# Kernel tuning notes

Hardware: AMD Instinct MI355X
Metric: run time of the kernel (lower is better)

Reference implementation:

```python
import jax, jax.numpy as jnp
import numpy as np

POOL = 7          # cf.pool_size
SR = 2            # roi_align sampling_ratio
LEVELS = [0, 1, 2, 3]
C = 192           # cf.end_filts
HC = 2            # cf.head_classes
RF = 1
N_ROIS = 1000
B = 4


def roi_align_2d(fmap, boxes, batch_inds, pool_size=POOL, sr=SR):
    """Bilinear RoIAlign. fmap [B,C,H,W]; boxes [N,4] = (y1,x1,y2,x2) in fmap pixel coords."""
    _, _, H, W = fmap.shape
    y1, x1, y2, x2 = boxes[:, 0], boxes[:, 1], boxes[:, 2], boxes[:, 3]
    bin_h = jnp.maximum(y2 - y1, 1.0) / pool_size
    bin_w = jnp.maximum(x2 - x1, 1.0) / pool_size
    # sampling offsets within the roi, [pool*sr]
    grid = (jnp.arange(pool_size, dtype=jnp.float32)[:, None]
            + (jnp.arange(sr, dtype=jnp.float32)[None, :] + 0.5) / sr).reshape(-1)
    ys = y1[:, None] + grid[None, :] * bin_h[:, None]   # [N, P*S]
    xs = x1[:, None] + grid[None, :] * bin_w[:, None]   # [N, P*S]
    y = jnp.broadcast_to(ys[:, :, None], (ys.shape[0], ys.shape[1], xs.shape[1]))  # [N,PS,PS]
    x = jnp.broadcast_to(xs[:, None, :], y.shape)
    valid = (y >= -1.0) & (y <= H) & (x >= -1.0) & (x <= W)
    y = jnp.clip(y, 0.0, H - 1)
    x = jnp.clip(x, 0.0, W - 1)
    y0 = jnp.floor(y).astype(jnp.int32)
    x0 = jnp.floor(x).astype(jnp.int32)
    y1i = jnp.minimum(y0 + 1, H - 1)
    x1i = jnp.minimum(x0 + 1, W - 1)
    ly = y - y0
    lx = x - x0
    b = batch_inds[:, None, None]
    f00 = fmap[b, :, y0, x0]    # [N,PS,PS,C]
    f01 = fmap[b, :, y0, x1i]
    f10 = fmap[b, :, y1i, x0]
    f11 = fmap[b, :, y1i, x1i]
    w00 = ((1 - ly) * (1 - lx))[..., None]
    w01 = ((1 - ly) * lx)[..., None]
    w10 = (ly * (1 - lx))[..., None]
    w11 = (ly * lx)[..., None]
    val = (f00 * w00 + f01 * w01 + f10 * w10 + f11 * w11) * valid[..., None]
    n = val.shape[0]
    val = val.reshape(n, pool_size, sr, pool_size, sr, -1).mean(axis=(2, 4))  # [N,P,P,C]
    return jnp.transpose(val, (0, 3, 1, 2))  # [N,C,P,P]


def pyramid_roi_align(fmaps, rois, pool_size=POOL, levels=LEVELS):
    boxes = jax.lax.stop_gradient(rois[:, :4])  # level_boxes.detach() in original
    batch_ix = rois[:, 4].astype(jnp.int32)
    h = boxes[:, 2] - boxes[:, 0]
    w = boxes[:, 3] - boxes[:, 1]
    roi_level = jnp.clip(jnp.round(4.0 + jnp.log2(jnp.sqrt(h * w))),
                         levels[0], levels[-1]).astype(jnp.int32)
    pooled = jnp.zeros((boxes.shape[0], fmaps[0].shape[1], pool_size, pool_size), fmaps[0].dtype)
    for li, lvl in enumerate(levels):
        H, W = fmaps[li].shape[2], fmaps[li].shape[3]
        scale = jnp.asarray([H, W, H, W], jnp.float32)
        p = roi_align_2d(fmaps[li], boxes * scale, batch_ix, pool_size)
        pooled = jnp.where((roi_level == lvl)[:, None, None, None], p, pooled)
    return pooled


def setup_inputs() -> dict:
    key = jax.random.key(0)
    ks = jax.random.split(key, 20)
    fmap0 = jax.random.normal(ks[0], (B, C, 128, 128), jnp.float32)
    fmap1 = jax.random.normal(ks[1], (B, C, 64, 64), jnp.float32)
    fmap2 = jax.random.normal(ks[2], (B, C, 32, 32), jnp.float32)
    fmap3 = jax.random.normal(ks[3], (B, C, 16, 16), jnp.float32)
    # valid normalized rois: (y1,x1,y2,x2,batch_ix)
    cy = jax.random.uniform(ks[4], (N_ROIS,), minval=0.15, maxval=0.85)
    cx = jax.random.uniform(ks[5], (N_ROIS,), minval=0.15, maxval=0.85)
    hh = jax.random.uniform(ks[6], (N_ROIS,), minval=0.02, maxval=0.15)
    hw = jax.random.uniform(ks[7], (N_ROIS,), minval=0.02, maxval=0.15)
    bix = jax.random.randint(ks[8], (N_ROIS,), 0, B).astype(jnp.float32)
    rois = jnp.stack([jnp.clip(cy - hh, 0, 1), jnp.clip(cx - hw, 0, 1),
                      jnp.clip(cy + hh, 0, 1), jnp.clip(cx + hw, 0, 1), bix], axis=1)
    d = C * 4  # 768
    s1 = 1.0 / np.sqrt(C * POOL * POOL)
    s2 = 1.0 / np.sqrt(d)
    params = dict(
        w1=jax.random.normal(ks[9], (d, C, POOL, POOL), jnp.float32) * s1,
        b1=jnp.zeros((d,), jnp.float32),
        w2=jax.random.normal(ks[10], (d, d), jnp.float32) * s2,
        b2=jnp.zeros((d,), jnp.float32),
        w_bbox=jax.random.normal(ks[11], (HC * 4, d), jnp.float32) * s2,
        b_bbox=jnp.zeros((HC * 4,), jnp.float32),
        w_cls=jax.random.normal(ks[12], (HC, d), jnp.float32) * s2,
        b_cls=jnp.zeros((HC,), jnp.float32),
        w_reg=jax.random.normal(ks[13], (HC * RF, d), jnp.float32) * s2,
        b_reg=jnp.zeros((HC * RF,), jnp.float32),
        w_unc=jax.random.normal(ks[14], (HC, d), jnp.float32) * s2,
        b_unc=jnp.zeros((HC,), jnp.float32),
    )
    return dict(fmap0=fmap0, fmap1=fmap1, fmap2=fmap2, fmap3=fmap3, rois=rois, **params)


def reference(fmap0, fmap1, fmap2, fmap3, rois, w1, b1, w2, b2,
              w_bbox, b_bbox, w_cls, b_cls, w_reg, b_reg, w_unc, b_unc):
    x = pyramid_roi_align([fmap0, fmap1, fmap2, fmap3], rois)      # [N,C,7,7]
    x = jax.nn.relu(jnp.einsum('ncij,ocij->no', x, w1) + b1)       # conv1 ks=7 -> 1x1
    x = jax.nn.relu(x @ w2.T + b2)                                 # conv2 1x1
    n = x.shape[0]
    mrcnn_bbox = (x @ w_bbox.T + b_bbox).reshape(n, -1, 4)         # [N,HC,2*dim]
    mrcnn_class_logits = x @ w_cls.T + b_cls                       # [N,HC]
    reg = (x @ w_reg.T + b_reg).reshape(n, -1, RF)
    unc = x @ w_unc.T + b_unc
    mrcnn_regress = jnp.concatenate([reg, unc[..., None]], axis=2)  # [N,HC,RF+1]
    return mrcnn_bbox, mrcnn_class_logits, mrcnn_regress
```

## Files before the change

### kernel.cpp

```cpp
#include <hip/hip_runtime.h>
#include <hip/hip_bf16.h>
#include <cstddef>
#include <cstdint>

typedef __attribute__((ext_vector_type(8))) short short8;
typedef __attribute__((ext_vector_type(16))) float float16;

#define C_CH 192
#define PK   9408
#define D1   768

__device__ __forceinline__ ushort f2bf(float v) {
    return __builtin_bit_cast(unsigned short, __float2bfloat16(v));
}

__device__ __forceinline__ void gload16(const void* g, void* l) {
    __builtin_amdgcn_global_load_lds(
        (const __attribute__((address_space(1))) void*)g,
        (__attribute__((address_space(3))) void*)l, 16, 0, 0);
}

__global__ __launch_bounds__(256) void cvt_bf16_2(
    const float* __restrict__ in1, ushort* __restrict__ out1, int n4_1,
    const float* __restrict__ in2, ushort* __restrict__ out2, int n4_2)
{
    int i = blockIdx.x * 256 + threadIdx.x;
    const float* in; ushort* out;
    if (i < n4_1) { in = in1; out = out1; }
    else          { i -= n4_1; if (i >= n4_2) return; in = in2; out = out2; }
    float4 v = ((const float4*)in)[i];
    ushort4 o;
    o.x = f2bf(v.x); o.y = f2bf(v.y); o.z = f2bf(v.z); o.w = f2bf(v.w);
    ((ushort4*)out)[i] = o;
}

__global__ __launch_bounds__(256) void cvt_bf16(const float* __restrict__ in,
                                                ushort* __restrict__ out, int n4)
{
    int i = blockIdx.x * 256 + threadIdx.x;
    if (i >= n4) return;
    float4 v = ((const float4*)in)[i];
    ushort4 o;
    o.x = f2bf(v.x); o.y = f2bf(v.y); o.z = f2bf(v.z); o.w = f2bf(v.w);
    ((ushort4*)out)[i] = o;
}

__global__ __launch_bounds__(256) void fused_pre(
    const float* __restrict__ f0, const float* __restrict__ f1,
    const float* __restrict__ f2, const float* __restrict__ f3,
    ushort* __restrict__ o0, ushort* __restrict__ o1,
    ushort* __restrict__ o2, ushort* __restrict__ o3,
    const float* __restrict__ w1src, ushort* __restrict__ w1dst, int n41,
    const float* __restrict__ w2src, ushort* __restrict__ w2dst, int n42,
    int nTrans)
{
    __shared__ unsigned int sm[96][33];

    int bx = blockIdx.x;
    if (bx >= nTrans) {
        int i = (bx - nTrans) * 256 + threadIdx.x;
        const float* in; ushort* out;
        if (i < n41) { in = w1src; out = w1dst; }
        else         { i -= n41; if (i >= n42) return; in = w2src; out = w2dst; }
        float4 v = ((const float4*)in)[i];
        ushort4 o;
        o.x = f2bf(v.x); o.y = f2bf(v.y); o.z = f2bf(v.z); o.w = f2bf(v.w);
        ((ushort4*)out)[i] = o;
        return;
    }

    int b = bx / 680;
    int t = bx - b * 680;
    const float* in; ushort* out; int HW, hw0;
    if      (t < 512) { in = f0; out = o0; HW = 16384; hw0 = t * 32; }
    else if (t < 640) { in = f1; out = o1; HW = 4096;  hw0 = (t - 512) * 32; }
    else if (t < 672) { in = f2; out = o2; HW = 1024;  hw0 = (t - 640) * 32; }
    else              { in = f3; out = o3; HW = 256;   hw0 = (t - 672) * 32; }

    int tx = threadIdx.x & 31;
    int ty = threadIdx.x >> 5;

    const float* ip = in + (size_t)b * C_CH * HW + hw0;
    #pragma unroll
    for (int it = 0; it < 12; ++it) {
        int cp = it * 8 + ty;
        float v0 = ip[(size_t)(2 * cp)     * HW + tx];
        float v1 = ip[(size_t)(2 * cp + 1) * HW + tx];
        sm[cp][tx] = (unsigned int)f2bf(v0) | ((unsigned int)f2bf(v1) << 16);
    }
    __syncthreads();

    unsigned int* op = (unsigned int*)(out + ((size_t)b * HW + hw0) * C_CH);
    #pragma unroll
    for (int it = 0; it < 12; ++it) {
        int idx = it * 256 + (int)threadIdx.x;
        int r = idx / 96;
        int p = idx - r * 96;
        op[idx] = sm[p][r];
    }
}

__device__ __forceinline__ void issue8(
    const char* sbase, const int (*offB)[4], int s2, int c16, float4* u)
{
    #pragma unroll
    for (int k = 0; k < 8; ++k) {
        int s  = s2 + (k >> 2);
        int tp = k & 3;
        u[k] = *(const float4*)(sbase + (offB[s][tp] + c16));
    }
}

__device__ __forceinline__ void comp8(
    const float4* u, const float (*wt)[4], int s2, float* a)
{
    #pragma unroll
    for (int k = 0; k < 8; ++k) {
        float w = wt[s2 + (k >> 2)][k & 3];
        unsigned int u0 = __builtin_bit_cast(unsigned int, u[k].x);
        unsigned int u1 = __builtin_bit_cast(unsigned int, u[k].y);
        unsigned int u2 = __builtin_bit_cast(unsigned int, u[k].z);
        unsigned int u3 = __builtin_bit_cast(unsigned int, u[k].w);
        a[0] = fmaf(__builtin_bit_cast(float, u0 << 16),         w, a[0]);
        a[1] = fmaf(__builtin_bit_cast(float, u0 & 0xffff0000u), w, a[1]);
        a[2] = fmaf(__builtin_bit_cast(float, u1 << 16),         w, a[2]);
        a[3] = fmaf(__builtin_bit_cast(float, u1 & 0xffff0000u), w, a[3]);
        a[4] = fmaf(__builtin_bit_cast(float, u2 << 16),         w, a[4]);
        a[5] = fmaf(__builtin_bit_cast(float, u2 & 0xffff0000u), w, a[5]);
        a[6] = fmaf(__builtin_bit_cast(float, u3 << 16),         w, a[6]);
        a[7] = fmaf(__builtin_bit_cast(float, u3 & 0xffff0000u), w, a[7]);
    }
}

__global__ __launch_bounds__(384, 3) void roi_gather(
    const ushort* __restrict__ n0p, const ushort* __restrict__ n1p,
    const ushort* __restrict__ n2p, const ushort* __restrict__ n3p,
    const float* __restrict__ rois, ushort* __restrict__ pooled)
{
    __shared__ int    s_offB[196][4];
    __shared__ float  s_w[196][4];
    __shared__ ushort s_out[PK];

    const int n   = blockIdx.x;
    const int tid = threadIdx.x;

    float by1 = rois[n*5+0], bx1 = rois[n*5+1];
    float by2 = rois[n*5+2], bx2 = rois[n*5+3];
    int   b   = (int)rois[n*5+4];

    float hh = by2 - by1, ww = bx2 - bx1;
    int lvl = (int)rintf(4.0f + log2f(sqrtf(hh * ww)));
    lvl = min(max(lvl, 0), 3);

    const ushort* fm; int H;
    if      (lvl == 0) { fm = n0p; H = 128; }
    else if (lvl == 1) { fm = n1p; H = 64;  }
    else if (lvl == 2) { fm = n2p; H = 32;  }
    else               { fm = n3p; H = 16;  }
    float Hf = (float)H;

    float y1p = by1 * Hf, x1p = bx1 * Hf;
    float y2p = by2 * Hf, x2p = bx2 * Hf;
    float bin_h = fmaxf(y2p - y1p, 1.0f) * (1.0f / 7.0f);
    float bin_w = fmaxf(x2p - x1p, 1.0f) * (1.0f / 7.0f);

    uintptr_t bp = (uintptr_t)(fm + (size_t)b * H * H * C_CH);
    unsigned int blo = __builtin_amdgcn_readfirstlane((unsigned int)bp);
    unsigned int bhi = __builtin_amdgcn_readfirstlane((unsigned int)(bp >> 32));
    const char* sbase = (const char*)((((uintptr_t)bhi) << 32) | blo);

    if (tid < 196) {
        int s = tid;
        int sx = s & 1, sy = (s >> 1) & 1, ij = s >> 2;
        int i = ij / 7, j = ij - i * 7;

        float gy = (float)i + 0.25f + 0.5f * (float)sy;
        float y  = y1p + gy * bin_h;
        bool  vy = (y >= -1.0f) && (y <= Hf);
        float yc = fminf(fmaxf(y, 0.0f), Hf - 1.0f);
        int   y0 = (int)floorf(yc);
        float ly = yc - (float)y0;
        int   y1i = min(y0 + 1, H - 1);

        float gx = (float)j + 0.25f + 0.5f * (float)sx;
        float x  = x1p + gx * bin_w;
        bool  vx = (x >= -1.0f) && (x <= Hf);
        float xc = fminf(fmaxf(x, 0.0f), Hf - 1.0f);
        int   x0 = (int)floorf(xc);
        float lx = xc - (float)x0;
        int   x1i = min(x0 + 1, H - 1);

        float vm = (vy && vx) ? 0.25f : 0.0f;
        s_offB[s][0] = (y0  * H + x0 ) * (C_CH * 2);
        s_offB[s][1] = (y0  * H + x1i) * (C_CH * 2);
        s_offB[s][2] = (y1i * H + x0 ) * (C_CH * 2);
        s_offB[s][3] = (y1i * H + x1i) * (C_CH * 2);
        s_w[s][0] = (1.0f - ly) * (1.0f - lx) * vm;
        s_w[s][1] = (1.0f - ly) * lx * vm;
        s_w[s][2] = ly * (1.0f - lx) * vm;
        s_w[s][3] = ly * lx * vm;
    }
    __syncthreads();

    const int grp = tid / 24;
    const int ci  = tid - grp * 24;
    const int cl  = ci * 8;
    const int c16 = ci * 16;
    const int bin_lo = (grp * 49) >> 4;
    const int bin_hi = ((grp + 1) * 49) >> 4;

    float4 ua[8], ub[8];
    float  a[8];

    issue8(sbase, s_offB, bin_lo * 4, c16, ua);
    for (int bin = bin_lo; bin < bin_hi; ++bin) {
        issue8(sbase, s_offB, bin * 4 + 2, c16, ub);
        #pragma unroll
        for (int k = 0; k < 8; ++k) a[k] = 0.0f;
        comp8(ua, s_w, bin * 4, a);
        if (bin + 1 < bin_hi)
            issue8(sbase, s_offB, (bin + 1) * 4, c16, ua);
        comp8(ub, s_w, bin * 4 + 2, a);
        #pragma unroll
        for (int k = 0; k < 8; ++k)
            s_out[(cl + k) * 49 + bin] = f2bf(a[k]);
    }
    __syncthreads();

    unsigned int* po = (unsigned int*)(pooled + (size_t)n * PK);
    const unsigned int* so = (const unsigned int*)s_out;
    for (int idx = tid; idx < PK / 2; idx += 384) po[idx] = so[idx];
}

__global__ __launch_bounds__(256) void roi_align_nchw(
    const float* __restrict__ f0, const float* __restrict__ f1,
    const float* __restrict__ f2, const float* __restrict__ f3,
    const float* __restrict__ rois, ushort* __restrict__ pooled, int n_rois)
{
    int idx = blockIdx.x * 256 + threadIdx.x;
    if (idx >= n_rois * PK) return;
    int n  = idx / PK;
    int r  = idx - n * PK;
    int c  = r / 49;
    int ij = r - c * 49;
    int i  = ij / 7;
    int j  = ij - i * 7;

    float by1 = rois[n*5+0], bx1 = rois[n*5+1];
    float by2 = rois[n*5+2], bx2 = rois[n*5+3];
    int   b   = (int)rois[n*5+4];

    float hh = by2 - by1, ww = bx2 - bx1;
    int lvl = (int)rintf(4.0f + log2f(sqrtf(hh * ww)));
    lvl = min(max(lvl, 0), 3);

    const float* fmap; int H;
    if      (lvl == 0) { fmap = f0; H = 128; }
    else if (lvl == 1) { fmap = f1; H = 64;  }
    else if (lvl == 2) { fmap = f2; H = 32;  }
    else               { fmap = f3; H = 16;  }
    float Hf = (float)H;

    float y1p = by1 * Hf, x1p = bx1 * Hf;
    float bin_h = fmaxf(by2 * Hf - y1p, 1.0f) * (1.0f / 7.0f);
    float bin_w = fmaxf(bx2 * Hf - x1p, 1.0f) * (1.0f / 7.0f);

    const float* base = fmap + ((size_t)b * C_CH + c) * (size_t)(H * H);

    float acc = 0.0f;
    #pragma unroll
    for (int sy = 0; sy < 2; ++sy) {
        float y  = y1p + ((float)i + 0.25f + 0.5f * (float)sy) * bin_h;
        bool  vy = (y >= -1.0f) && (y <= Hf);
        float yc = fminf(fmaxf(y, 0.0f), Hf - 1.0f);
        int   y0 = (int)floorf(yc);
        float ly = yc - (float)y0;
        int   y1i = min(y0 + 1, H - 1);
        #pragma unroll
        for (int sx = 0; sx < 2; ++sx) {
            float x  = x1p + ((float)j + 0.25f + 0.5f * (float)sx) * bin_w;
            bool  vx = (x >= -1.0f) && (x <= Hf);
            float xc = fminf(fmaxf(x, 0.0f), Hf - 1.0f);
            int   x0 = (int)floorf(xc);
            float lx = xc - (float)x0;
            int   x1i = min(x0 + 1, H - 1);
            if (vy && vx) {
                float v = base[y0 * H + x0 ] * (1.0f - ly) * (1.0f - lx)
                        + base[y0 * H + x1i] * (1.0f - ly) * lx
                        + base[y1i * H + x0 ] * ly * (1.0f - lx)
                        + base[y1i * H + x1i] * ly * lx;
                acc += v;
            }
        }
    }
    pooled[idx] = f2bf(acc * 0.25f);
}

template<int MODE>
__global__ __launch_bounds__(256) void mfma_gemm(
    const ushort* __restrict__ A, const ushort* __restrict__ W,
    const float* __restrict__ bias, void* __restrict__ outp,
    int M, int N, int K, int nkPer, int nkTotal)
{
    __shared__ char ldsA[2][8192];
    __shared__ char ldsB[2][8192];

    const int t    = threadIdx.x;
    const int lane = t & 63;
    const int wave = t >> 6;
    const int wm = wave >> 1, wn = wave & 1;

    const int m0 = blockIdx.y * 64;
    const int n0 = blockIdx.x * 64;
    const int kb = (MODE == 2) ? blockIdx.z * nkPer : 0;
    const int nk = (MODE == 2) ? min(nkPer, nkTotal - kb) : nkPer;

    const int ks   = t & 3;
    const int mrow = t >> 2;
    const int g    = mrow >> 5;
    const int rw   = mrow & 31;
    const int lof0 = ks*2048 + g*1024 + ((     rw) ^ (ks<<2))*16;
    const int lof1 = ks*2048 + g*1024 + ((32 + rw) ^ (ks<<2))*16;

    const int arow = min(m0 + mrow, M-1);
    const int brow = n0 + mrow;
    const ushort* ap = A + (size_t)arow * K + (size_t)kb * 64 + ks*16;
    const ushort* bp = W + (size_t)brow * K + (size_t)kb * 64 + ks*16;

    float4 ra0, ra1, rb0, rb1;
    float4 qa0, qa1, qb0, qb1;

    ra0 = ((const float4*)ap)[0]; ra1 = ((const float4*)ap)[1];
    rb0 = ((const float4*)bp)[0]; rb1 = ((const float4*)bp)[1];
    *(float4*)&ldsA[0][lof0] = ra0; *(float4*)&ldsA[0][lof1] = ra1;
    *(float4*)&ldsB[0][lof0] = rb0; *(float4*)&ldsB[0][lof1] = rb1;
    {
        int k1 = min(1, nk - 1);
        const ushort* ap1 = ap + (size_t)k1 * 64;
        const ushort* bp1 = bp + (size_t)k1 * 64;
        ra0 = ((const float4*)ap1)[0]; ra1 = ((const float4*)ap1)[1];
        rb0 = ((const float4*)bp1)[0]; rb1 = ((const float4*)bp1)[1];
    }
    __syncthreads();

    float16 acc = {};

    for (int kt = 0; kt < nk; ++kt) {
        {
            int k2 = min(kt + 2, nk - 1);
            const ushort* ap2 = ap + (size_t)k2 * 64;
            const ushort* bp2 = bp + (size_t)k2 * 64;
            qa0 = ((const float4*)ap2)[0]; qa1 = ((const float4*)ap2)[1];
            qb0 = ((const float4*)bp2)[0]; qb1 = ((const float4*)bp2)[1];
        }
        if (kt + 1 < nk) {
            char* dA = ldsA[(kt+1)&1]; char* dB = ldsB[(kt+1)&1];
            *(float4*)&dA[lof0] = ra0; *(float4*)&dA[lof1] = ra1;
            *(float4*)&dB[lof0] = rb0; *(float4*)&dB[lof1] = rb1;
        }
        const char* sA = ldsA[kt&1]; const char* sB = ldsB[kt&1];
        #pragma unroll
        for (int s = 0; s < 4; ++s) {
            int ro = s*2048 + (lane ^ (s<<2))*16;
            short8 af = *(const short8*)&sA[wm*1024 + ro];
            short8 bf = *(const short8*)&sB[wn*1024 + ro];
            acc = __builtin_amdgcn_mfma_f32_32x32x16_bf16(af, bf, acc, 0, 0, 0);
        }
        __syncthreads();
        ra0 = qa0; ra1 = qa1; rb0 = qb0; rb1 = qb1;
    }

    const int col   = lane & 31;
    const int rbase = 4 * (lane >> 5);
    const int nG    = n0 + wn*32 + col;

    if (MODE == 2) {
        float* O = (float*)outp + (size_t)blockIdx.z * M * N;
        #pragma unroll
        for (int r = 0; r < 16; ++r) {
            int row = (r & 3) + 8*(r >> 2) + rbase;
            int mG  = m0 + wm*32 + row;
            if (mG < M) O[(size_t)mG * N + nG] = acc[r];
        }
    } else if (MODE == 1) {
        const float bv = bias[nG];
        ushort* O = (ushort*)outp;
        #pragma unroll
        for (int r = 0; r < 16; ++r) {
            int row = (r & 3) + 8*(r >> 2) + rbase;
            int mG  = m0 + wm*32 + row;
            if (mG < M) O[(size_t)mG * N + nG] = f2bf(fmaxf(acc[r] + bv, 0.0f));
        }
    } else {
        const float bv = bias[nG];
        float* O = (float*)outp;
        #pragma unroll
        for (int r = 0; r < 16; ++r) {
            int row = (r & 3) + 8*(r >> 2) + rbase;
            int mG  = m0 + wm*32 + row;
            if (mG < M) O[(size_t)mG * N + nG] = fmaxf(acc[r] + bv, 0.0f);
        }
    }
}

__global__ __launch_bounds__(256) void mfma_gemm128(
    const ushort* __restrict__ A, const ushort* __restrict__ W,
    void* __restrict__ outp, int M, int N, int K, int nkPer, int nkTotal)
{
    __shared__ char ldsA[2][16384];
    __shared__ char ldsB[2][16384];

    const int t    = threadIdx.x;
    const int lane = t & 63;
    const int wave = t >> 6;
    const int wm = wave >> 1, wn = wave & 1;

    const int m0 = blockIdx.y * 128;
    const int n0 = blockIdx.x * 128;
    const int kb = blockIdx.z * nkPer;
    const int nk = min(nkPer, nkTotal - kb);

    int aoff[4], boff[4], lofs[4];
    #pragma unroll
    for (int i = 0; i < 4; ++i) {
        int sid = wave * 4 + i;
        int ks = sid >> 2, h = (sid >> 1) & 1, g = sid & 1;
        int swz = ks << 2;
        int rl  = h * 64 + g * 32 + ((lane & 31) ^ swz);
        int ko  = ks * 16 + (lane >> 5) * 8;
        int arow = min(m0 + rl, M - 1);
        int brow = n0 + rl;
        aoff[i] = arow * K + ko;
        boff[i] = brow * K + ko;
        lofs[i] = sid * 1024;
    }
    const size_t kbase = (size_t)kb * 64;

    #define STAGE128(buf, kt)                                                  \
        do {                                                                   \
            const ushort* Ab_ = A + kbase + (size_t)(kt) * 64;                 \
            const ushort* Wb_ = W + kbase + (size_t)(kt) * 64;                 \
            _Pragma("unroll")                                                  \
            for (int i_ = 0; i_ < 4; ++i_) {                                   \
                gload16(Ab_ + aoff[i_], &ldsA[buf][lofs[i_]]);                 \
                gload16(Wb_ + boff[i_], &ldsB[buf][lofs[i_]]);                 \
            }                                                                  \
        } while (0)

    STAGE128(0, 0);
    __syncthreads();

    float16 acc00 = {}, acc01 = {}, acc10 = {}, acc11 = {};

    for (int kt = 0; kt < nk; ++kt) {
        if (kt + 1 < nk) STAGE128((kt + 1) & 1, kt + 1);
        const char* sA = ldsA[kt & 1];
        const char* sB = ldsB[kt & 1];
        #pragma unroll
        for (int s = 0; s < 4; ++s) {
            int ro = s*4096 + (lane ^ (s<<2))*16;
            short8 a0 = *(const short8*)&sA[wm*2048        + ro];
            short8 a1 = *(const short8*)&sA[wm*2048 + 1024 + ro];
            short8 b0 = *(const short8*)&sB[wn*2048        + ro];
            short8 b1 = *(const short8*)&sB[wn*2048 + 1024 + ro];
            acc00 = __builtin_amdgcn_mfma_f32_32x32x16_bf16(a0, b0, acc00, 0, 0, 0);
            acc01 = __builtin_amdgcn_mfma_f32_32x32x16_bf16(a0, b1, acc01, 0, 0, 0);
            acc10 = __builtin_amdgcn_mfma_f32_32x32x16_bf16(a1, b0, acc10, 0, 0, 0);
            acc11 = __builtin_amdgcn_mfma_f32_32x32x16_bf16(a1, b1, acc11, 0, 0, 0);
        }
        __syncthreads();
    }
    #undef STAGE128

    const int col   = lane & 31;
    const int rbase = 4 * (lane >> 5);
    float* O = (float*)outp + (size_t)blockIdx.z * M * N;

    const int mb0 = m0 + wm*64;
    const int nb0 = n0 + wn*64;
    #pragma unroll
    for (int r = 0; r < 16; ++r) {
        int row = (r & 3) + 8*(r >> 2) + rbase;
        int mG0 = mb0 + row;
        int mG1 = mb0 + 32 + row;
        int nG0 = nb0 + col;
        int nG1 = nb0 + 32 + col;
        if (mG0 < M) {
            O[(size_t)mG0 * N + nG0] = acc00[r];
            O[(size_t)mG0 * N + nG1] = acc01[r];
        }
        if (mG1 < M) {
            O[(size_t)mG1 * N + nG0] = acc10[r];
            O[(size_t)mG1 * N + nG1] = acc11[r];
        }
    }
}

__global__ __launch_bounds__(256) void reduce_relu_bf16(
    const float* __restrict__ P, const float* __restrict__ bias,
    ushort* __restrict__ Y, int MN, int N, int S)
{
    int idx = blockIdx.x * 256 + threadIdx.x;
    if (idx >= MN / 4) return;
    float4 s = ((const float4*)P)[idx];
    for (int k = 1; k < S; ++k) {
        float4 p = ((const float4*)(P + (size_t)k * MN))[idx];
        s.x += p.x; s.y += p.y; s.z += p.z; s.w += p.w;
    }
    int n4 = idx % (N / 4);
    float4 bv = ((const float4*)bias)[n4];
    ushort4 o;
    o.x = f2bf(fmaxf(s.x + bv.x, 0.0f));
    o.y = f2bf(fmaxf(s.y + bv.y, 0.0f));
    o.z = f2bf(fmaxf(s.z + bv.z, 0.0f));
    o.w = f2bf(fmaxf(s.w + bv.w, 0.0f));
    ((ushort4*)Y)[idx] = o;
}

__global__ __launch_bounds__(256) void reduce_heads(
    const float* __restrict__ P2, const float* __restrict__ b2, int S, int MN,
    const float* __restrict__ w_bbox, const float* __restrict__ b_bbox,
    const float* __restrict__ w_cls,  const float* __restrict__ b_cls,
    const float* __restrict__ w_reg,  const float* __restrict__ b_reg,
    const float* __restrict__ w_unc,  const float* __restrict__ b_unc,
    float* __restrict__ out, int n_rois)
{
    __shared__ float zrow[D1];
    const int m   = blockIdx.x;
    const int tid = threadIdx.x;

    const float* Pm = P2 + (size_t)m * D1;
    #pragma unroll
    for (int r = 0; r < 3; ++r) {
        int k = r * 256 + tid;
        float v = Pm[k];
        for (int s = 1; s < S; ++s) v += Pm[(size_t)s * MN + k];
        zrow[k] = fmaxf(v + b2[k], 0.0f);
    }
    __syncthreads();

    const int wave = tid >> 6;
    const int lane = tid & 63;
    for (int o = wave; o < 14; o += 4) {
        const float* w; float bb;
        if      (o < 8)  { w = w_bbox + o * D1;        bb = b_bbox[o]; }
        else if (o < 10) { w = w_cls  + (o - 8) * D1;  bb = b_cls[o - 8]; }
        else if (o < 12) { w = w_reg  + (o - 10) * D1; bb = b_reg[o - 10]; }
        else             { w = w_unc  + (o - 12) * D1; bb = b_unc[o - 12]; }
        float p = 0.0f;
        #pragma unroll
        for (int r = 0; r < 12; ++r) {
            int k = r * 64 + lane;
            p = fmaf(zrow[k], w[k], p);
        }
        #pragma unroll
        for (int d = 32; d >= 1; d >>= 1) p += __shfl_down(p, d, 64);
        if (lane == 0) {
            int off;
            int clsOff = n_rois * 8;
            int regOff = n_rois * 10;
            if      (o < 8)  off = m * 8 + o;
            else if (o < 10) off = clsOff + m * 2 + (o - 8);
            else if (o < 12) off = regOff + m * 4 + (o - 10) * 2;
            else             off = regOff + m * 4 + (o - 12) * 2 + 1;
            out[off] = p + bb;
        }
    }
}

__global__ __launch_bounds__(256) void heads_kernel(
    const float* __restrict__ Z,
    const float* __restrict__ w_bbox, const float* __restrict__ b_bbox,
    const float* __restrict__ w_cls,  const float* __restrict__ b_cls,
    const float* __restrict__ w_reg,  const float* __restrict__ b_reg,
    const float* __restrict__ w_unc,  const float* __restrict__ b_unc,
    float* __restrict__ out, int n_rois)
{
    int idx = blockIdx.x * 256 + threadIdx.x;
    if (idx >= n_rois * 14) return;
    int n = idx / 14;
    int o = idx - n * 14;

    const float* w; float bb;
    if      (o < 8)  { w = w_bbox + o * D1;        bb = b_bbox[o]; }
    else if (o < 10) { w = w_cls  + (o - 8) * D1;  bb = b_cls[o - 8]; }
    else if (o < 12) { w = w_reg  + (o - 10) * D1; bb = b_reg[o - 10]; }
    else             { w = w_unc  + (o - 12) * D1; bb = b_unc[o - 12]; }

    const float* z = Z + (size_t)n * D1;
    float s = bb;
    for (int k = 0; k < D1; k += 4) {
        float4 zv = *(const float4*)(z + k);
        float4 wv = *(const float4*)(w + k);
        s = fmaf(zv.x, wv.x, s);
        s = fmaf(zv.y, wv.y, s);
        s = fmaf(zv.z, wv.z, s);
        s = fmaf(zv.w, wv.w, s);
    }

    int off;
    int clsOff = n_rois * 8;
    int regOff = n_rois * 10;
    if      (o < 8)  off = n * 8 + o;
    else if (o < 10) off = clsOff + n * 2 + (o - 8);
    else if (o < 12) off = regOff + n * 4 + (o - 10) * 2;
    else             off = regOff + n * 4 + (o - 12) * 2 + 1;
    out[off] = s;
}

extern "C" void kernel_launch(void* const* d_in, const int* in_sizes, int n_in,
                              void* d_out, int out_size, void* d_ws, size_t ws_size,
                              hipStream_t stream)
{
    const float* f0   = (const float*)d_in[0];
    const float* f1   = (const float*)d_in[1];
    const float* f2   = (const float*)d_in[2];
    const float* f3   = (const float*)d_in[3];
    const float* rois = (const float*)d_in[4];
    const float* w1   = (const float*)d_in[5];
    const float* b1   = (const float*)d_in[6];
    const float* w2   = (const float*)d_in[7];
    const float* b2   = (const float*)d_in[8];
    const float* w_bbox = (const float*)d_in[9];
    const float* b_bbox = (const float*)d_in[10];
    const float* w_cls  = (const float*)d_in[11];
    const float* b_cls  = (const float*)d_in[12];
    const float* w_reg  = (const float*)d_in[13];
    const float* b_reg  = (const float*)d_in[14];
    const float* w_unc  = (const float*)d_in[15];
    const float* b_unc  = (const float*)d_in[16];
    float* out = (float*)d_out;

    const int n_rois = in_sizes[4] / 5;
    const int B      = in_sizes[0] / (C_CH * 128 * 128);

    const size_t nh0B = (size_t)B * 16384 * C_CH * 2;
    const size_t nh1B = (size_t)B * 4096  * C_CH * 2;
    const size_t nh2B = (size_t)B * 1024  * C_CH * 2;
    const size_t nh3B = (size_t)B * 256   * C_CH * 2;
    const size_t nhAll = nh0B + nh1B + nh2B + nh3B;
    const size_t poolB = (size_t)n_rois * PK * 2;
    const size_t w1Bb  = (size_t)D1 * PK * 2;
    const size_t w2Bb  = (size_t)D1 * D1 * 2;
    const size_t Yb    = (size_t)n_rois * D1 * 2;
    const size_t Zb    = (size_t)n_rois * D1 * 4;
    const size_t smallB = w2Bb + Yb + Zb;

    const int SPLIT1  = 10;
    const int SPLIT1F = 5;
    const int SPLIT2  = 2;

    const size_t P1b   = (size_t)SPLIT1 * n_rois * D1 * 4;
    const size_t needX2 = nhAll + poolB + w1Bb + w2Bb + Yb;
    const size_t needX  = nhAll + poolB + smallB;

    char* ws = (char*)d_ws;

    int n41 = D1*PK/4, n42 = D1*D1/4;

    if (ws_size >= needX2) {
        ushort* nh0 = (ushort*)ws;
        ushort* nh1 = nh0 + nh0B/2;
        ushort* nh2 = nh1 + nh1B/2;
        ushort* nh3 = nh2 + nh2B/2;
        ushort* pooledB = (ushort*)(ws + nhAll);
        ushort* w1B = (ushort*)(ws + nhAll + poolB);
        ushort* w2B = (ushort*)(ws + nhAll + poolB + w1Bb);
        ushort* Y   = (ushort*)(ws + nhAll + poolB + w1Bb + w2Bb);
        float*  P   = (float*)ws;
        float*  P2  = (float*)(ws + P1b);

        int nTrans = 680 * B;
        int nCvt   = (n41 + n42 + 255) / 256;
        fused_pre<<<nTrans + nCvt, 256, 0, stream>>>(
            f0, f1, f2, f3, nh0, nh1, nh2, nh3,
            w1, w1B, n41, w2, w2B, n42, nTrans);

        roi_gather<<<n_rois, 384, 0, stream>>>(nh0, nh1, nh2, nh3, rois, pooledB);

        {
            int nkTotal = PK / 64;
            int nkPer   = (nkTotal + SPLIT1 - 1) / SPLIT1;
            dim3 grid(D1/128, (n_rois + 127)/128, SPLIT1);
            mfma_gemm128<<<grid, 256, 0, stream>>>(pooledB, w1B, P,
                                                   n_rois, D1, PK, nkPer, nkTotal);
            int MN = n_rois * D1;
            reduce_relu_bf16<<<(MN/4 + 255)/256, 256, 0, stream>>>(P, b1, Y, MN, D1, SPLIT1);
        }
        {
            int nkTotal = D1 / 64;
            int nkPer   = nkTotal / SPLIT2;
            dim3 grid(D1/64, (n_rois + 63)/64, SPLIT2);
            mfma_gemm<2><<<grid, 256, 0, stream>>>(Y, w2B, nullptr, P2,
                                                   n_rois, D1, D1, nkPer, nkTotal);
            int MN = n_rois * D1;
            reduce_heads<<<n_rois, 256, 0, stream>>>(P2, b2, SPLIT2, MN,
                w_bbox, b_bbox, w_cls, b_cls, w_reg, b_reg, w_unc, b_unc, out, n_rois);
        }
    } else if (ws_size >= needX) {
        ushort* nh0 = (ushort*)ws;
        ushort* nh1 = nh0 + nh0B/2;
        ushort* nh2 = nh1 + nh1B/2;
        ushort* nh3 = nh2 + nh2B/2;
        ushort* w1B = (ushort*)ws;
        float*  P   = (float*)(ws + w1Bb);
        float*  P2  = (float*)ws;
        ushort* pooledB = (ushort*)(ws + nhAll);
        ushort* w2B = (ushort*)(ws + nhAll + poolB);
        ushort* Y   = w2B + w2Bb/2;

        int nTrans = 680 * B;
        fused_pre<<<nTrans, 256, 0, stream>>>(
            f0, f1, f2, f3, nh0, nh1, nh2, nh3,
            w1, (ushort*)nullptr, 0, w2, (ushort*)nullptr, 0, nTrans);
        roi_gather<<<n_rois, 384, 0, stream>>>(nh0, nh1, nh2, nh3, rois, pooledB);
        cvt_bf16_2<<<(n41 + n42 + 255)/256, 256, 0, stream>>>(
            w1, w1B, n41, w2, w2B, n42);
        {
            int nkTotal = PK / 64;
            int nkPer   = (nkTotal + SPLIT1F - 1) / SPLIT1F;
            dim3 grid(D1/64, (n_rois + 63)/64, SPLIT1F);
            mfma_gemm<2><<<grid, 256, 0, stream>>>(pooledB, w1B, nullptr, P,
                                                   n_rois, D1, PK, nkPer, nkTotal);
            int MN = n_rois * D1;
            reduce_relu_bf16<<<(MN/4 + 255)/256, 256, 0, stream>>>(P, b1, Y, MN, D1, SPLIT1F);
        }
        {
            int nkTotal = D1 / 64;
            int nkPer   = nkTotal / SPLIT2;
            dim3 grid(D1/64, (n_rois + 63)/64, SPLIT2);
            mfma_gemm<2><<<grid, 256, 0, stream>>>(Y, w2B, nullptr, P2,
                                                   n_rois, D1, D1, nkPer, nkTotal);
            int MN = n_rois * D1;
            reduce_heads<<<n_rois, 256, 0, stream>>>(P2, b2, SPLIT2, MN,
                w_bbox, b_bbox, w_cls, b_cls, w_reg, b_reg, w_unc, b_unc, out, n_rois);
        }
    } else {
        ushort* pooledB = (ushort*)ws;
        ushort* w1B = pooledB + poolB/2;
        ushort* w2B = w1B + w1Bb/2;
        ushort* Y   = w2B + w2Bb/2;
        float*  Z   = (float*)((char*)Y + Yb);

        cvt_bf16<<<((D1*PK/4) + 255)/256, 256, 0, stream>>>(w1, w1B, D1*PK/4);
        cvt_bf16<<<((D1*D1/4) + 255)/256, 256, 0, stream>>>(w2, w2B, D1*D1/4);
        {
            int total = n_rois * PK;
            roi_align_nchw<<<(total + 255)/256, 256, 0, stream>>>(
                f0, f1, f2, f3, rois, pooledB, n_rois);
        }
        {
            dim3 grid(D1/64, (n_rois + 63)/64);
            mfma_gemm<1><<<grid, 256, 0, stream>>>(pooledB, w1B, b1, Y,
                                                   n_rois, D1, PK, PK/64, PK/64);
        }
        {
            dim3 grid(D1/64, (n_rois + 63)/64);
            mfma_gemm<0><<<grid, 256, 0, stream>>>(Y, w2B, b2, Z,
                                                   n_rois, D1, D1, D1/64, D1/64);
        }
        heads_kernel<<<(n_rois*14 + 255)/256, 256, 0, stream>>>(
            Z, w_bbox, b_bbox, w_cls, b_cls, w_reg, b_reg, w_unc, b_unc, out, n_rois);
    }
}
```

Before: 229.4 us.

## Separate RoIAlign bilinear weights per axis and merge duplicate sample taps

Bilinear weights are now built separately for the y and x axes of each bin. Taps that land on the same row or column index are merged and zero-weight taps are dropped, so each bin gathers only its distinct pixels, up to 16 per bin instead of always 16 loads. This should cut redundant global loads for small RoIs. It gives up the software double-buffered prefetch across bins and adds data-dependent loop bounds, which may serialize load latency.

```diff
diff --git a/kernel.cpp b/kernel.cpp
--- a/kernel.cpp
+++ b/kernel.cpp
@@ -100,45 +100,14 @@
     }
 }
 
-__device__ __forceinline__ void issue8(
-    const char* sbase, const int (*offB)[4], int s2, int c16, float4* u)
-{
-    #pragma unroll
-    for (int k = 0; k < 8; ++k) {
-        int s  = s2 + (k >> 2);
-        int tp = k & 3;
-        u[k] = *(const float4*)(sbase + (offB[s][tp] + c16));
-    }
-}
-
-__device__ __forceinline__ void comp8(
-    const float4* u, const float (*wt)[4], int s2, float* a)
-{
-    #pragma unroll
-    for (int k = 0; k < 8; ++k) {
-        float w = wt[s2 + (k >> 2)][k & 3];
-        unsigned int u0 = __builtin_bit_cast(unsigned int, u[k].x);
-        unsigned int u1 = __builtin_bit_cast(unsigned int, u[k].y);
-        unsigned int u2 = __builtin_bit_cast(unsigned int, u[k].z);
-        unsigned int u3 = __builtin_bit_cast(unsigned int, u[k].w);
-        a[0] = fmaf(__builtin_bit_cast(float, u0 << 16),         w, a[0]);
-        a[1] = fmaf(__builtin_bit_cast(float, u0 & 0xffff0000u), w, a[1]);
-        a[2] = fmaf(__builtin_bit_cast(float, u1 << 16),         w, a[2]);
-        a[3] = fmaf(__builtin_bit_cast(float, u1 & 0xffff0000u), w, a[3]);
-        a[4] = fmaf(__builtin_bit_cast(float, u2 << 16),         w, a[4]);
-        a[5] = fmaf(__builtin_bit_cast(float, u2 & 0xffff0000u), w, a[5]);
-        a[6] = fmaf(__builtin_bit_cast(float, u3 << 16),         w, a[6]);
-        a[7] = fmaf(__builtin_bit_cast(float, u3 & 0xffff0000u), w, a[7]);
-    }
-}
-
 __global__ __launch_bounds__(384, 3) void roi_gather(
     const ushort* __restrict__ n0p, const ushort* __restrict__ n1p,
     const ushort* __restrict__ n2p, const ushort* __restrict__ n3p,
     const float* __restrict__ rois, ushort* __restrict__ pooled)
 {
-    __shared__ int    s_offB[196][4];
-    __shared__ float  s_w[196][4];
+    __shared__ int    s_off[49][2][4];
+    __shared__ float  s_wt [49][2][4];
+    __shared__ int    s_cnt[49][2];
     __shared__ ushort s_out[PK];
 
     const int n   = blockIdx.x;
@@ -169,36 +138,45 @@
     unsigned int bhi = __builtin_amdgcn_readfirstlane((unsigned int)(bp >> 32));
     const char* sbase = (const char*)((((uintptr_t)bhi) << 32) | blo);
 
-    if (tid < 196) {
-        int s = tid;
-        int sx = s & 1, sy = (s >> 1) & 1, ij = s >> 2;
-        int i = ij / 7, j = ij - i * 7;
-
-        float gy = (float)i + 0.25f + 0.5f * (float)sy;
-        float y  = y1p + gy * bin_h;
-        bool  vy = (y >= -1.0f) && (y <= Hf);
-        float yc = fminf(fmaxf(y, 0.0f), Hf - 1.0f);
-        int   y0 = (int)floorf(yc);
-        float ly = yc - (float)y0;
-        int   y1i = min(y0 + 1, H - 1);
-
-        float gx = (float)j + 0.25f + 0.5f * (float)sx;
-        float x  = x1p + gx * bin_w;
-        bool  vx = (x >= -1.0f) && (x <= Hf);
-        float xc = fminf(fmaxf(x, 0.0f), Hf - 1.0f);
-        int   x0 = (int)floorf(xc);
-        float lx = xc - (float)x0;
-        int   x1i = min(x0 + 1, H - 1);
-
-        float vm = (vy && vx) ? 0.25f : 0.0f;
-        s_offB[s][0] = (y0  * H + x0 ) * (C_CH * 2);
-        s_offB[s][1] = (y0  * H + x1i) * (C_CH * 2);
-        s_offB[s][2] = (y1i * H + x0 ) * (C_CH * 2);
-        s_offB[s][3] = (y1i * H + x1i) * (C_CH * 2);
-        s_w[s][0] = (1.0f - ly) * (1.0f - lx) * vm;
-        s_w[s][1] = (1.0f - ly) * lx * vm;
-        s_w[s][2] = ly * (1.0f - lx) * vm;
-        s_w[s][3] = ly * lx * vm;
+    if (tid < 98) {
+        int bin = tid >> 1, dim = tid & 1;
+        int bi  = bin / 7, bj = bin - bi * 7;
+        int pos   = dim ? bj : bi;
+        float org = dim ? x1p : y1p;
+        float bsz = dim ? bin_w : bin_h;
+
+        int   idxs[4];
+        float wts[4];
+        int   cnt = 0;
+        #pragma unroll
+        for (int s = 0; s < 2; ++s) {
+            float g  = (float)pos + 0.25f + 0.5f * (float)s;
+            float v  = org + g * bsz;
+            bool  ok = (v >= -1.0f) && (v <= Hf);
+            float vc = fminf(fmaxf(v, 0.0f), Hf - 1.0f);
+            int   p0 = (int)floorf(vc);
+            float l  = vc - (float)p0;
+            int   p1 = min(p0 + 1, H - 1);
+            float w0 = ok ? 0.5f * (1.0f - l) : 0.0f;
+            float w1 = ok ? 0.5f * l          : 0.0f;
+            #pragma unroll
+            for (int e = 0; e < 2; ++e) {
+                int   pi = e ? p1 : p0;
+                float wi = e ? w1 : w0;
+                if (wi != 0.0f) {
+                    bool merged = false;
+                    for (int k = 0; k < cnt; ++k)
+                        if (idxs[k] == pi) { wts[k] += wi; merged = true; break; }
+                    if (!merged) { idxs[cnt] = pi; wts[cnt] = wi; ++cnt; }
+                }
+            }
+        }
+        int stride = dim ? (C_CH * 2) : (H * C_CH * 2);
+        for (int k = 0; k < cnt; ++k) {
+            s_off[bin][dim][k] = idxs[k] * stride;
+            s_wt [bin][dim][k] = wts[k];
+        }
+        s_cnt[bin][dim] = cnt;
     }
     __syncthreads();
 
@@ -209,18 +187,37 @@
     const int bin_lo = (grp * 49) >> 4;
     const int bin_hi = ((grp + 1) * 49) >> 4;
 
-    float4 ua[8], ub[8];
-    float  a[8];
-
-    issue8(sbase, s_offB, bin_lo * 4, c16, ua);
     for (int bin = bin_lo; bin < bin_hi; ++bin) {
-        issue8(sbase, s_offB, bin * 4 + 2, c16, ub);
+        const int nr = s_cnt[bin][0];
+        const int nc = s_cnt[bin][1];
+        float a[8];
         #pragma unroll
         for (int k = 0; k < 8; ++k) a[k] = 0.0f;
-        comp8(ua, s_w, bin * 4, a);
-        if (bin + 1 < bin_hi)
-            issue8(sbase, s_offB, (bin + 1) * 4, c16, ua);
-        comp8(ub, s_w, bin * 4 + 2, a);
+
+        #pragma unroll
+        for (int r = 0; r < 4; ++r) {
+            if (r >= nr) break;
+            const char* rp = sbase + (s_off[bin][0][r] + c16);
+            const float rw = s_wt[bin][0][r];
+            #pragma unroll
+            for (int c = 0; c < 4; ++c) {
+                if (c >= nc) break;
+                float4 u = *(const float4*)(rp + s_off[bin][1][c]);
+                float  w = rw * s_wt[bin][1][c];
+                unsigned int u0 = __builtin_bit_cast(unsigned int, u.x);
+                unsigned int u1 = __builtin_bit_cast(unsigned int, u.y);
+                unsigned int u2 = __builtin_bit_cast(unsigned int, u.z);
+                unsigned int u3 = __builtin_bit_cast(unsigned int, u.w);
+                a[0] = fmaf(__builtin_bit_cast(float, u0 << 16),         w, a[0]);
+                a[1] = fmaf(__builtin_bit_cast(float, u0 & 0xffff0000u), w, a[1]);
+                a[2] = fmaf(__builtin_bit_cast(float, u1 << 16),         w, a[2]);
+                a[3] = fmaf(__builtin_bit_cast(float, u1 & 0xffff0000u), w, a[3]);
+                a[4] = fmaf(__builtin_bit_cast(float, u2 << 16),         w, a[4]);
+                a[5] = fmaf(__builtin_bit_cast(float, u2 & 0xffff0000u), w, a[5]);
+                a[6] = fmaf(__builtin_bit_cast(float, u3 << 16),         w, a[6]);
+                a[7] = fmaf(__builtin_bit_cast(float, u3 & 0xffff0000u), w, a[7]);
+            }
+        }
         #pragma unroll
         for (int k = 0; k < 8; ++k)
             s_out[(cl + k) * 49 + bin] = f2bf(a[k]);
```

New measurement: 227.4 us, median of 2. About the same (-0.9%).
